# Kernel optimization log

Hardware: AMD Instinct MI355X
Metric: run time of the kernel (lower is better)

## Reference

```python
import jax, jax.numpy as jnp
import numpy as np

N = 50000      # nodes
E_R = 800000   # random edges (plus N self-loops appended)
F = 128        # input feature dim
HD = 256       # base hidden dim
D = 64         # gnn_dim (per-head out channels)
H = 4          # attention heads
A = 32         # n_actions
LEAKY = 0.2    # PyG GATv2 negative_slope default
LN_EPS = 1e-5


def _ln(x, g, b):
    mu = x.mean(-1, keepdims=True)
    v = ((x - mu) ** 2).mean(-1, keepdims=True)
    return (x - mu) / jnp.sqrt(v + LN_EPS) * g + b


def _gatv2(x, src, dst, wl, wr, att, wres, bias):
    # GATv2Conv, concat=False (mean over heads), residual=True, no edge_attr.
    xl = (x @ wl).reshape(-1, H, D)   # [N,H,D] source transform
    xr = (x @ wr).reshape(-1, H, D)   # [N,H,D] target transform
    m = jax.nn.leaky_relu(xl[src] + xr[dst], LEAKY)          # [E,H,D]
    e = jnp.einsum('ehd,hd->eh', m, att)                     # [E,H]
    emax = jax.ops.segment_max(e, dst, num_segments=N)       # [N,H]
    p = jnp.exp(e - emax[dst])
    denom = jax.ops.segment_sum(p, dst, num_segments=N)      # [N,H]
    alpha = p / denom[dst]                                   # segment softmax
    out = jax.ops.segment_sum(alpha[..., None] * xl[src], dst, num_segments=N)
    out = out.mean(axis=1)                                   # concat=False -> head mean
    return out + x @ wres + bias                             # residual + bias


def setup_inputs() -> dict:
    key = jax.random.key(0)
    ks = jax.random.split(key, 16)
    inputs = jax.random.normal(ks[0], (N, F), jnp.float32)
    src_r = jax.random.randint(ks[1], (E_R,), 0, N, jnp.int32)
    dst_r = jax.random.randint(ks[2], (E_R,), 0, N, jnp.int32)
    loops = jnp.arange(N, dtype=jnp.int32)  # add_self_loops=True default in PyG
    src = jnp.concatenate([src_r, loops])
    dst = jnp.concatenate([dst_r, loops])
    w = lambda k, s: jax.random.normal(k, s, jnp.float32) * 0.05
    return {
        'inputs': inputs, 'src': src, 'dst': dst,
        'w0': w(ks[3], (F, HD)), 'b0': jnp.zeros((HD,)), 'g0': jnp.ones((HD,)), 'be0': jnp.zeros((HD,)),
        'w1': w(ks[4], (HD, HD)), 'b1': jnp.zeros((HD,)), 'g1': jnp.ones((HD,)), 'be1': jnp.zeros((HD,)),
        'wl1': w(ks[5], (HD, H * D)), 'wr1': w(ks[6], (HD, H * D)), 'att1': w(ks[7], (H, D)),
        'wres1': w(ks[8], (HD, D)), 'bias1': jnp.zeros((D,)), 'lg1': jnp.ones((D,)), 'lb1': jnp.zeros((D,)),
        'wl2': w(ks[9], (D, H * D)), 'wr2': w(ks[10], (D, H * D)), 'att2': w(ks[11], (H, D)),
        'wres2': w(ks[12], (D, D)), 'bias2': jnp.zeros((D,)), 'lg2': jnp.ones((D,)), 'lb2': jnp.zeros((D,)),
        'wa': w(ks[13], (D, A)), 'ba': jnp.zeros((A,)),
    }


def reference(inputs, src, dst, w0, b0, g0, be0, w1, b1, g1, be1,
              wl1, wr1, att1, wres1, bias1, lg1, lb1,
              wl2, wr2, att2, wres2, bias2, lg2, lb2, wa, ba):
    # base MLP: (Linear + ReLU + LayerNorm) x 2
    x = _ln(jax.nn.relu(inputs @ w0 + b0), g0, be0)
    x = _ln(jax.nn.relu(x @ w1 + b1), g1, be1)
    # GATv2 stack: (GATv2Conv + ReLU + LayerNorm) x 2
    h = _ln(jax.nn.relu(_gatv2(x, src, dst, wl1, wr1, att1, wres1, bias1)), lg1, lb1)
    h = _ln(jax.nn.relu(_gatv2(h, src, dst, wl2, wr2, att2, wres2, bias2)), lg2, lb2)
    q = h @ wa + ba
    return q
```

## Files before the change

### kernel.cpp

```cpp
#include <hip/hip_runtime.h>
#include <stdint.h>

#define LEAKY 0.2f
#define LN_EPS 1e-5f
#define BF16_ONES 0x3F803F80u

extern "C" __global__ void GNNAgentV2_84834194031328_kernel() {}

typedef __attribute__((ext_vector_type(8))) short short8;
typedef __attribute__((ext_vector_type(4))) float f32x4;

__device__ __forceinline__ float bfbits2f(uint32_t bits){
    union { uint32_t u; float f; } c; c.u = bits; return c.f;
}
__device__ __forceinline__ float bf2f(uint16_t u){ return bfbits2f(((uint32_t)u) << 16); }
__device__ __forceinline__ uint16_t f2bf(float f){
    union { float f; uint32_t u; } c; c.f = f;
    uint32_t u = c.u;
    return (uint16_t)((u + 0x7fffu + ((u >> 16) & 1u)) >> 16);
}
__device__ __forceinline__ void ld_bf16x4(const uint16_t* p, float* o){
    uint2 v = *(const uint2*)p;
    o[0] = bfbits2f(v.x << 16);
    o[1] = bfbits2f(v.x & 0xffff0000u);
    o[2] = bfbits2f(v.y << 16);
    o[3] = bfbits2f(v.y & 0xffff0000u);
}
__device__ __forceinline__ void st_bf16x4(uint16_t* p, float a, float b, float c, float d){
    uint2 v;
    v.x = (uint32_t)f2bf(a) | ((uint32_t)f2bf(b) << 16);
    v.y = (uint32_t)f2bf(c) | ((uint32_t)f2bf(d) << 16);
    *(uint2*)p = v;
}

template<int CTRL>
__device__ __forceinline__ float dpp_add(float v){
    int x = __builtin_amdgcn_update_dpp(0, __builtin_bit_cast(int, v), CTRL, 0xF, 0xF, true);
    return v + __builtin_bit_cast(float, x);
}

struct Seg { const void* src; uint16_t* dst; int K; int N; int colOff; };
struct SegTable { Seg s[22]; };

__global__ void k_front(SegTable st, const uint32_t* __restrict__ g0w,
                        const int* __restrict__ dst, int* __restrict__ counts, int E, int nbE,
                        const void* __restrict__ xin, uint16_t* __restrict__ xout, int nin)
{
    int b = blockIdx.x;
    if (b < nbE){
        int e = b * 256 + threadIdx.x;
        if (e < E) atomicAdd(&counts[dst[e]], 1);
        return;
    }
    b -= nbE;
    if (b < 22 * 256){
        int isbf = (*g0w == BF16_ONES) ? 1 : 0;
        Seg sg = st.s[b >> 8];
        int elems = sg.K * sg.N;
        int idx = (b & 255) * 256 + threadIdx.x;
        if (idx >= elems) return;
        float v = isbf ? bf2f(((const uint16_t*)sg.src)[idx]) : ((const float*)sg.src)[idx];
        if (sg.K == 1){
            sg.dst[idx] = f2bf(v);
            return;
        }
        int k = idx / sg.N, c = idx - k * sg.N;
        int cg = sg.colOff + c;
        int ct = cg >> 6, c64 = cg & 63;
        int cf = c64 >> 4, l15 = c64 & 15;
        int kf = k >> 5, r = k & 31;
        int quad = r >> 3, j = r & 7;
        size_t off = (size_t)ct * sg.K * 64 + kf * 2048 + cf * 512 + (quad * 16 + l15) * 8 + j;
        sg.dst[off] = f2bf(v);
        return;
    }
    b -= 22 * 256;
    {
        if (*g0w == BF16_ONES) return;
        int i = b * 256 + threadIdx.x;
        if (i < nin) xout[i] = f2bf(((const float*)xin)[i]);
    }
}

__global__ void k_scan1(const int* __restrict__ counts, int* __restrict__ offs,
                        int* __restrict__ bsums, int n){
    __shared__ int sd[256];
    int t = threadIdx.x;
    int base = blockIdx.x * 1024 + t * 4;
    int v0 = (base + 0 < n) ? counts[base + 0] : 0;
    int v1 = (base + 1 < n) ? counts[base + 1] : 0;
    int v2 = (base + 2 < n) ? counts[base + 2] : 0;
    int v3 = (base + 3 < n) ? counts[base + 3] : 0;
    int tsum = v0 + v1 + v2 + v3;
    sd[t] = tsum;
    __syncthreads();
    for (int off = 1; off < 256; off <<= 1){
        int x = 0;
        if (t >= off) x = sd[t - off];
        __syncthreads();
        sd[t] += x;
        __syncthreads();
    }
    int run = sd[t] - tsum;
    if (base + 0 < n){ offs[base + 0] = run; } run += v0;
    if (base + 1 < n){ offs[base + 1] = run; } run += v1;
    if (base + 2 < n){ offs[base + 2] = run; } run += v2;
    if (base + 3 < n){ offs[base + 3] = run; }
    if (t == 255) bsums[blockIdx.x] = sd[255];
}
__global__ void k_scan23(const int* __restrict__ bsums, int* __restrict__ offs,
                         int* __restrict__ cursor, int n){
    int lane = threadIdx.x & 63;
    int idx = blockIdx.x >> 2;
    int total = 0;
    for (int base = 0; base < idx; base += 64){
        int v = (base + lane < idx) ? bsums[base + lane] : 0;
        v += __shfl_xor(v, 1);  v += __shfl_xor(v, 2);  v += __shfl_xor(v, 4);
        v += __shfl_xor(v, 8);  v += __shfl_xor(v, 16); v += __shfl_xor(v, 32);
        total += v;
    }
    int i = blockIdx.x * 256 + threadIdx.x;
    if (i < n){
        int o = offs[i] + total;
        offs[i] = o;
        cursor[i] = o;
    }
}
__global__ void k_scatter(const int* __restrict__ src, const int* __restrict__ dst,
                          int* __restrict__ cursor, int* __restrict__ csr_src, int E){
    int e = blockIdx.x * 256 + threadIdx.x;
    if (e < E){
        int p = atomicAdd(&cursor[dst[e]], 1);
        csr_src[p] = src[e];
    }
}

template<int K, int CG, bool BIAS_RELU>
__global__ __launch_bounds__(256, 4) void k_gemm(
    const uint16_t* __restrict__ A,
    const uint16_t* __restrict__ Bp,
    const uint16_t* __restrict__ bias,
    uint16_t* __restrict__ o0, int ld0,
    uint16_t* __restrict__ o1, int ld1,
    uint16_t* __restrict__ o2, int ld2,
    int s1, int s2,
    int n,
    const uint32_t* __restrict__ g0w, int want)
{
    if (want >= 0){
        int isbf = (*g0w == BF16_ONES) ? 1 : 0;
        if (isbf != want) return;
    }
    constexpr int PITCH = K + 8;
    __shared__ __align__(16) uint16_t SMEM[64 * PITCH];
    uint16_t* As = SMEM;
    uint16_t* Cs = SMEM;
    int t = threadIdx.x;
    int row0 = blockIdx.x * 64;
    int ctBase = blockIdx.y * CG;

    constexpr int KC = K / 8;
    for (int c = t; c < 64 * KC; c += 256){
        int r = c / KC, kc = c - r * KC;
        uint4 v = make_uint4(0, 0, 0, 0);
        int gr = row0 + r;
        if (gr < n) v = *(const uint4*)(A + (size_t)gr * K + kc * 8);
        *(uint4*)(As + r * PITCH + kc * 8) = v;
    }

    int lane = t & 63, wv = t >> 6;
    int quad = lane >> 4, l15 = lane & 15;
    int wrow = wv * 16;

    __syncthreads();

    constexpr int KF = K / 32;
    short8 areg[KF];
    #pragma unroll
    for (int kf = 0; kf < KF; ++kf)
        areg[kf] = __builtin_bit_cast(short8,
            *(const uint4*)(As + (wrow + l15) * PITCH + kf * 32 + quad * 8));

    __syncthreads();

    for (int g = 0; g < CG; ++g){
        int ct = ctBase + g;
        const uint16_t* Bb = Bp + (size_t)ct * K * 64 + (size_t)lane * 8;

        f32x4 acc[4];
        #pragma unroll
        for (int j = 0; j < 4; ++j) acc[j] = (f32x4){0.f, 0.f, 0.f, 0.f};

        short8 bcur[4], bnxt[4];
        #pragma unroll
        for (int cf = 0; cf < 4; ++cf)
            bcur[cf] = __builtin_bit_cast(short8, *(const uint4*)(Bb + cf * 512));

        #pragma unroll
        for (int kf = 0; kf < KF; ++kf){
            if (kf + 1 < KF){
                #pragma unroll
                for (int cf = 0; cf < 4; ++cf)
                    bnxt[cf] = __builtin_bit_cast(short8,
                        *(const uint4*)(Bb + (kf + 1) * 2048 + cf * 512));
            }
            #pragma unroll
            for (int cf = 0; cf < 4; ++cf)
                acc[cf] = __builtin_amdgcn_mfma_f32_16x16x32_bf16(areg[kf], bcur[cf], acc[cf], 0, 0, 0);
            if (kf + 1 < KF){
                #pragma unroll
                for (int cf = 0; cf < 4; ++cf) bcur[cf] = bnxt[cf];
            }
        }

        #pragma unroll
        for (int r = 0; r < 4; ++r){
            #pragma unroll
            for (int cf = 0; cf < 4; ++cf){
                float v = acc[cf][r];
                if (BIAS_RELU){
                    v += bf2f(bias[ct * 64 + cf * 16 + l15]);
                    v = v > 0.f ? v : 0.f;
                }
                Cs[(wrow + quad * 4 + r) * 72 + cf * 16 + l15] = f2bf(v);
            }
        }
        __syncthreads();

        uint16_t* obase; int ld, colOut;
        if (ct < s1)      { obase = o0; ld = ld0; colOut = ct * 64; }
        else if (ct < s2) { obase = o1; ld = ld1; colOut = (ct - s1) * 64; }
        else              { obase = o2; ld = ld2; colOut = (ct - s2) * 64; }

        for (int i = t; i < 512; i += 256){
            int row = i >> 3, sg = i & 7;
            int grow = row0 + row;
            if (grow < n){
                uint4 v = *(const uint4*)(Cs + row * 72 + sg * 8);
                *(uint4*)(obase + (size_t)grow * ld + colOut + sg * 8) = v;
            }
        }
        __syncthreads();
    }
}

__global__ __launch_bounds__(256) void k_ln256(
    uint16_t* __restrict__ x, const uint16_t* __restrict__ g,
    const uint16_t* __restrict__ be, int n)
{
    int t = threadIdx.x;
    int lane = t & 63, wv = t >> 6;
    int row = blockIdx.x * 8 + wv * 2;
    int c0 = lane * 4;
    float gv[4], bev[4];
    ld_bf16x4(g + c0, gv);
    ld_bf16x4(be + c0, bev);
    #pragma unroll
    for (int rr = 0; rr < 2; ++rr){
        int r = row + rr;
        if (r >= n) continue;
        float v[4];
        ld_bf16x4(x + (size_t)r * 256 + c0, v);
        float s1 = v[0] + v[1] + v[2] + v[3];
        float s2 = v[0]*v[0] + v[1]*v[1] + v[2]*v[2] + v[3]*v[3];
        #pragma unroll
        for (int m = 1; m < 64; m <<= 1){
            s1 += __shfl_xor(s1, m);
            s2 += __shfl_xor(s2, m);
        }
        float mean = s1 * (1.f / 256.f);
        float var  = s2 * (1.f / 256.f) - mean * mean;
        float rstd = rsqrtf(var + LN_EPS);
        st_bf16x4(x + (size_t)r * 256 + c0,
                  (v[0] - mean) * rstd * gv[0] + bev[0],
                  (v[1] - mean) * rstd * gv[1] + bev[1],
                  (v[2] - mean) * rstd * gv[2] + bev[2],
                  (v[3] - mean) * rstd * gv[3] + bev[3]);
    }
}

__global__ __launch_bounds__(128) void k_gat_aggregate(
    const uint16_t* __restrict__ xl, const uint16_t* __restrict__ xr,
    const uint16_t* __restrict__ res,
    const uint16_t* __restrict__ att,
    const uint16_t* __restrict__ bias,
    const uint16_t* __restrict__ lg, const uint16_t* __restrict__ lb,
    const int* __restrict__ offs, const int* __restrict__ counts, const int* __restrict__ csr_src,
    uint16_t* __restrict__ out, int n)
{
    int node = __builtin_amdgcn_readfirstlane((blockIdx.x << 1) + (threadIdx.x >> 6));
    if (node >= n) return;
    int lane = threadIdx.x & 63;
    int c0 = lane * 4;
    float xr4[4], av[4];
    ld_bf16x4(xr + (size_t)node * 256 + c0, xr4);
    ld_bf16x4(att + c0, av);
    int start = offs[node], cnt = counts[node];
    float lsum = 0.f;
    float a0 = 0.f, a1 = 0.f, a2 = 0.f, a3 = 0.f;

    #define EDGE_SCORE(x, e)                                             \
    {                                                                    \
        float u0 = x[0] + xr4[0]; u0 = fmaxf(u0, LEAKY * u0);            \
        float u1 = x[1] + xr4[1]; u1 = fmaxf(u1, LEAKY * u1);            \
        float u2 = x[2] + xr4[2]; u2 = fmaxf(u2, LEAKY * u2);            \
        float u3 = x[3] + xr4[3]; u3 = fmaxf(u3, LEAKY * u3);            \
        e = u0 * av[0] + u1 * av[1] + u2 * av[2] + u3 * av[3];           \
    }
    #define REDUCE16(e)                                                  \
        e = dpp_add<0xB1>(e);                                            \
        e = dpp_add<0x4E>(e);                                            \
        e = dpp_add<0x141>(e);                                           \
        e = dpp_add<0x140>(e);

    int j = 0;
    if (cnt >= 4){
        int i0 = csr_src[start + 0];
        int i1 = csr_src[start + 1];
        int i2 = csr_src[start + 2];
        int i3 = csr_src[start + 3];
        while (true){
            int t0 = __builtin_amdgcn_readfirstlane(i0);
            int t1 = __builtin_amdgcn_readfirstlane(i1);
            int t2 = __builtin_amdgcn_readfirstlane(i2);
            int t3 = __builtin_amdgcn_readfirstlane(i3);
            int jn = j + 4;
            bool more = (jn + 3 < cnt);
            if (more){
                i0 = csr_src[start + jn + 0];
                i1 = csr_src[start + jn + 1];
                i2 = csr_src[start + jn + 2];
                i3 = csr_src[start + jn + 3];
            }
            float x0[4], x1[4], x2[4], x3[4];
            ld_bf16x4(xl + (size_t)(uint32_t)t0 * 256 + c0, x0);
            ld_bf16x4(xl + (size_t)(uint32_t)t1 * 256 + c0, x1);
            ld_bf16x4(xl + (size_t)(uint32_t)t2 * 256 + c0, x2);
            ld_bf16x4(xl + (size_t)(uint32_t)t3 * 256 + c0, x3);
            float e0, e1, e2, e3;
            EDGE_SCORE(x0, e0); EDGE_SCORE(x1, e1); EDGE_SCORE(x2, e2); EDGE_SCORE(x3, e3);
            REDUCE16(e0); REDUCE16(e1); REDUCE16(e2); REDUCE16(e3);
            float p0 = __expf(e0);
            float p1 = __expf(e1);
            float p2 = __expf(e2);
            float p3 = __expf(e3);
            a0 += p0*x0[0] + p1*x1[0] + p2*x2[0] + p3*x3[0];
            a1 += p0*x0[1] + p1*x1[1] + p2*x2[1] + p3*x3[1];
            a2 += p0*x0[2] + p1*x1[2] + p2*x2[2] + p3*x3[2];
            a3 += p0*x0[3] + p1*x1[3] + p2*x2[3] + p3*x3[3];
            lsum += p0 + p1 + p2 + p3;
            j = jn;
            if (!more) break;
        }
    }
    for (; j < cnt; ++j){
        int t0 = __builtin_amdgcn_readfirstlane(csr_src[start + j]);
        float x0[4];
        ld_bf16x4(xl + (size_t)(uint32_t)t0 * 256 + c0, x0);
        float e0;
        EDGE_SCORE(x0, e0);
        REDUCE16(e0);
        float p0 = __expf(e0);
        a0 += p0 * x0[0];
        a1 += p0 * x0[1];
        a2 += p0 * x0[2];
        a3 += p0 * x0[3];
        lsum += p0;
    }
    #undef EDGE_SCORE
    #undef REDUCE16

    float inv = 1.f / lsum;
    a0 *= inv; a1 *= inv; a2 *= inv; a3 *= inv;
    a0 += __shfl_xor(a0, 16); a0 += __shfl_xor(a0, 32);
    a1 += __shfl_xor(a1, 16); a1 += __shfl_xor(a1, 32);
    a2 += __shfl_xor(a2, 16); a2 += __shfl_xor(a2, 32);
    a3 += __shfl_xor(a3, 16); a3 += __shfl_xor(a3, 32);
    a0 *= 0.25f; a1 *= 0.25f; a2 *= 0.25f; a3 *= 0.25f;
    int d0 = (lane & 15) * 4;
    float r4[4], bvv[4];
    ld_bf16x4(res + (size_t)node * 64 + d0, r4);
    ld_bf16x4(bias + d0, bvv);
    float v0 = a0 + r4[0] + bvv[0]; v0 = v0 > 0.f ? v0 : 0.f;
    float v1 = a1 + r4[1] + bvv[1]; v1 = v1 > 0.f ? v1 : 0.f;
    float v2 = a2 + r4[2] + bvv[2]; v2 = v2 > 0.f ? v2 : 0.f;
    float v3 = a3 + r4[3] + bvv[3]; v3 = v3 > 0.f ? v3 : 0.f;
    float s1 = v0 + v1 + v2 + v3;
    float s2 = v0*v0 + v1*v1 + v2*v2 + v3*v3;
    s1 += __shfl_xor(s1, 1); s2 += __shfl_xor(s2, 1);
    s1 += __shfl_xor(s1, 2); s2 += __shfl_xor(s2, 2);
    s1 += __shfl_xor(s1, 4); s2 += __shfl_xor(s2, 4);
    s1 += __shfl_xor(s1, 8); s2 += __shfl_xor(s2, 8);
    float mean = s1 * (1.f / 64.f);
    float var  = s2 * (1.f / 64.f) - mean * mean;
    float rstd = rsqrtf(var + LN_EPS);
    if (lane < 16){
        float gvv[4], bev[4];
        ld_bf16x4(lg + d0, gvv);
        ld_bf16x4(lb + d0, bev);
        st_bf16x4(out + (size_t)node * 64 + d0,
                  (v0 - mean) * rstd * gvv[0] + bev[0],
                  (v1 - mean) * rstd * gvv[1] + bev[1],
                  (v2 - mean) * rstd * gvv[2] + bev[2],
                  (v3 - mean) * rstd * gvv[3] + bev[3]);
    }
}

__global__ __launch_bounds__(256) void k_final(
    const uint16_t* __restrict__ h, const void* __restrict__ wa,
    const void* __restrict__ ba, void* __restrict__ out, int n,
    const uint32_t* __restrict__ g0w)
{
    __shared__ float was[64][32];
    __shared__ float bas[32];
    __shared__ float hs[8][64];
    int t = threadIdx.x;
    int isbf = (*g0w == BF16_ONES) ? 1 : 0;
    for (int i = t; i < 64 * 32; i += 256)
        was[i >> 5][i & 31] = isbf ? bf2f(((const uint16_t*)wa)[i]) : ((const float*)wa)[i];
    if (t < 32) bas[t] = isbf ? bf2f(((const uint16_t*)ba)[t]) : ((const float*)ba)[t];
    int row0 = blockIdx.x * 8;
    for (int i = t; i < 8 * 64; i += 256){
        int r = i >> 6, k = i & 63;
        int rr = row0 + r;
        hs[r][k] = (rr < n) ? bf2f(h[(size_t)rr * 64 + k]) : 0.f;
    }
    __syncthreads();
    int r = t >> 5, c = t & 31;
    float acc = bas[c];
    #pragma unroll
    for (int k = 0; k < 64; ++k) acc += hs[r][k] * was[k][c];
    int node = row0 + r;
    if (node < n){
        if (isbf) ((uint16_t*)out)[(size_t)node * 32 + c] = f2bf(acc);
        else      ((float*)out)[(size_t)node * 32 + c] = acc;
    }
}

extern "C" void kernel_launch(void* const* d_in, const int* in_sizes, int n_in,
                              void* d_out, int out_size, void* d_ws, size_t ws_size,
                              hipStream_t stream)
{
    const int* src = (const int*)d_in[1];
    const int* dst = (const int*)d_in[2];
    const uint32_t* g0w = (const uint32_t*)d_in[5];
    const int N = in_sizes[0] / 128;
    const int E = in_sizes[1];

    char* base = (char*)d_ws;
    size_t off = 0;
    auto alloc = [&](size_t bytes) -> void* {
        void* p = base + off;
        off += (bytes + 255) & ~(size_t)255;
        return p;
    };
    uint16_t* XIN  = (uint16_t*)alloc((size_t)N * 128 * 2);
    uint16_t* X0   = (uint16_t*)alloc((size_t)N * 256 * 2);
    uint16_t* X1   = (uint16_t*)alloc((size_t)N * 256 * 2);
    uint16_t* XL   = (uint16_t*)alloc((size_t)N * 256 * 2);
    uint16_t* XR   = (uint16_t*)alloc((size_t)N * 256 * 2);
    uint16_t* RES  = (uint16_t*)alloc((size_t)N * 64 * 2);
    uint16_t* w0P  = (uint16_t*)alloc(256 * 128 * 2);
    uint16_t* w1P  = (uint16_t*)alloc(256 * 256 * 2);
    uint16_t* wt1P = (uint16_t*)alloc(576 * 256 * 2);
    uint16_t* wt2P = (uint16_t*)alloc(576 * 64 * 2);
    uint16_t* VEC  = (uint16_t*)alloc(4096 * 2);
    int* counts    = (int*)alloc((size_t)N * 4);
    int* offs      = (int*)alloc((size_t)N * 4);
    int* cursor    = (int*)alloc((size_t)N * 4);
    int* bsums     = (int*)alloc(4096);
    int* csr_src   = (int*)alloc((size_t)E * 4);

    uint16_t* H1 = X0;
    uint16_t* H2 = X0 + (size_t)N * 64;

    const int vB0=0, vG0=256, vBE0=512, vB1=768, vG1=1024, vBE1=1280;
    const int vATT1=1536, vBIAS1=1792, vLG1=1856, vLB1=1920;
    const int vATT2=1984, vBIAS2=2240, vLG2=2304, vLB2=2368;

    SegTable st;
    int si = 0;
    auto seg = [&](int i, uint16_t* d, int K, int Nn, int colOff){
        st.s[si++] = { d_in[i], d, K, Nn, colOff };
    };
    seg(3,  w0P, 128, 256, 0);
    seg(7,  w1P, 256, 256, 0);
    seg(11, wt1P, 256, 256, 0);
    seg(12, wt1P, 256, 256, 256);
    seg(14, wt1P, 256, 64, 512);
    seg(18, wt2P, 64, 256, 0);
    seg(19, wt2P, 64, 256, 256);
    seg(21, wt2P, 64, 64, 512);
    seg(4,  VEC+vB0, 1, 256, 0);  seg(5,  VEC+vG0, 1, 256, 0);  seg(6,  VEC+vBE0, 1, 256, 0);
    seg(8,  VEC+vB1, 1, 256, 0);  seg(9,  VEC+vG1, 1, 256, 0);  seg(10, VEC+vBE1, 1, 256, 0);
    seg(13, VEC+vATT1, 1, 256, 0); seg(15, VEC+vBIAS1, 1, 64, 0);
    seg(16, VEC+vLG1, 1, 64, 0);   seg(17, VEC+vLB1, 1, 64, 0);
    seg(20, VEC+vATT2, 1, 256, 0); seg(22, VEC+vBIAS2, 1, 64, 0);
    seg(23, VEC+vLG2, 1, 64, 0);   seg(24, VEC+vLB2, 1, 64, 0);

    const int nin = N * 128;
    const int nbE = (E + 255) / 256;
    const int nbI = (nin + 255) / 256;
    const int nb_scan  = (N + 1023) / 1024;
    const int nb_nodes = (N + 255) / 256;

    hipMemsetAsync(counts, 0, (size_t)N * 4, stream);
    k_front<<<nbE + 22 * 256 + nbI, 256, 0, stream>>>(
        st, g0w, dst, counts, E, nbE, d_in[0], XIN, nin);

    k_scan1<<<nb_scan, 256, 0, stream>>>(counts, offs, bsums, N);
    k_scan23<<<nb_nodes, 256, 0, stream>>>(bsums, offs, cursor, N);
    k_scatter<<<nbE, 256, 0, stream>>>(src, dst, cursor, csr_src, E);

    const int rt = (N + 63) / 64;
    const int nb_ln  = (N + 7) / 8;
    const int nb_agg = (N + 1) / 2;

    k_gemm<128, 4, true><<<rt, 256, 0, stream>>>(
        (const uint16_t*)d_in[0], w0P, VEC+vB0, X0,256, X0,256, X0,256, 99, 99, N, g0w, 1);
    k_gemm<128, 4, true><<<rt, 256, 0, stream>>>(
        XIN, w0P, VEC+vB0, X0,256, X0,256, X0,256, 99, 99, N, g0w, 0);
    k_ln256<<<nb_ln, 256, 0, stream>>>(X0, VEC+vG0, VEC+vBE0, N);
    k_gemm<256, 4, true><<<rt, 256, 0, stream>>>(
        X0, w1P, VEC+vB1, X1,256, X1,256, X1,256, 99, 99, N, nullptr, -1);
    k_ln256<<<nb_ln, 256, 0, stream>>>(X1, VEC+vG1, VEC+vBE1, N);

    k_gemm<256, 9, false><<<rt, 256, 0, stream>>>(
        X1, wt1P, nullptr, XL,256, XR,256, RES,64, 4, 8, N, nullptr, -1);
    k_gat_aggregate<<<nb_agg, 128, 0, stream>>>(XL, XR, RES,
        VEC+vATT1, VEC+vBIAS1, VEC+vLG1, VEC+vLB1, offs, counts, csr_src, H1, N);

    k_gemm<64, 9, false><<<rt, 256, 0, stream>>>(
        H1, wt2P, nullptr, XL,256, XR,256, RES,64, 4, 8, N, nullptr, -1);
    k_gat_aggregate<<<nb_agg, 128, 0, stream>>>(XL, XR, RES,
        VEC+vATT2, VEC+vBIAS2, VEC+vLG2, VEC+vLB2, offs, counts, csr_src, H2, N);

    k_final<<<nb_ln, 256, 0, stream>>>(H2, d_in[25], d_in[26], d_out, N, g0w);
}
```

Measured before the change: 497.0 us.

## Store GAT projections as fp16 and compute edge scores with packed fp16 dot2

The projection GEMMs now write XL/XR/RES in fp16 instead of bf16. The aggregation kernel computes leaky-relu and the attention dot product with packed half2 math and fdot2. In the 4-edge loop, the four per-edge 16-lane reductions are merged into one DPP transpose-and-reduce, so a single exp serves all four edges, and the results are broadcast back with DPP quad permutes. This is meant to cut VALU work and DPP and exp instruction count in the latency-bound gather loop. In exchange it loses range relative to bf16, which risks overflow if projected values get large.

Result: faster. 485.0 us (-2.4%).

```diff
diff --git a/kernel.cpp b/kernel.cpp
--- a/kernel.cpp
+++ b/kernel.cpp
@@ -9,6 +9,7 @@
 
 typedef __attribute__((ext_vector_type(8))) short short8;
 typedef __attribute__((ext_vector_type(4))) float f32x4;
+typedef _Float16 f16x2 __attribute__((ext_vector_type(2)));
 
 __device__ __forceinline__ float bfbits2f(uint32_t bits){
     union { uint32_t u; float f; } c; c.u = bits; return c.f;
@@ -19,6 +20,11 @@
     uint32_t u = c.u;
     return (uint16_t)((u + 0x7fffu + ((u >> 16) & 1u)) >> 16);
 }
+__device__ __forceinline__ uint16_t f2h(float f){
+    _Float16 h = (_Float16)f;
+    return __builtin_bit_cast(uint16_t, h);
+}
+__device__ __forceinline__ f16x2 u2h2(uint32_t u){ return __builtin_bit_cast(f16x2, u); }
 __device__ __forceinline__ void ld_bf16x4(const uint16_t* p, float* o){
     uint2 v = *(const uint2*)p;
     o[0] = bfbits2f(v.x << 16);
@@ -33,10 +39,24 @@
     *(uint2*)p = v;
 }
 
+__device__ __forceinline__ float dot2acc(f16x2 a, f16x2 b, float c){
+#if __has_builtin(__builtin_amdgcn_fdot2)
+    return __builtin_amdgcn_fdot2(a, b, c, false);
+#else
+    c = fmaf((float)a.x, (float)b.x, c);
+    return fmaf((float)a.y, (float)b.y, c);
+#endif
+}
+
 template<int CTRL>
 __device__ __forceinline__ float dpp_add(float v){
     int x = __builtin_amdgcn_update_dpp(0, __builtin_bit_cast(int, v), CTRL, 0xF, 0xF, true);
     return v + __builtin_bit_cast(float, x);
+}
+template<int CTRL>
+__device__ __forceinline__ float dpp_mov(float v){
+    int x = __builtin_amdgcn_update_dpp(0, __builtin_bit_cast(int, v), CTRL, 0xF, 0xF, true);
+    return __builtin_bit_cast(float, x);
 }
 
 struct Seg { const void* src; uint16_t* dst; int K; int N; int colOff; };
@@ -135,7 +155,7 @@
     }
 }
 
-template<int K, int CG, bool BIAS_RELU>
+template<int K, int CG, bool BIAS_RELU, bool OUT_F16>
 __global__ __launch_bounds__(256, 4) void k_gemm(
     const uint16_t* __restrict__ A,
     const uint16_t* __restrict__ Bp,
@@ -222,7 +242,7 @@
                     v += bf2f(bias[ct * 64 + cf * 16 + l15]);
                     v = v > 0.f ? v : 0.f;
                 }
-                Cs[(wrow + quad * 4 + r) * 72 + cf * 16 + l15] = f2bf(v);
+                Cs[(wrow + quad * 4 + r) * 72 + cf * 16 + l15] = OUT_F16 ? f2h(v) : f2bf(v);
             }
         }
         __syncthreads();
@@ -292,26 +312,25 @@
     if (node >= n) return;
     int lane = threadIdx.x & 63;
     int c0 = lane * 4;
-    float xr4[4], av[4];
-    ld_bf16x4(xr + (size_t)node * 256 + c0, xr4);
+    uint2 xrv = *(const uint2*)(xr + (size_t)node * 256 + c0);
+    f16x2 xr0 = u2h2(xrv.x), xr1 = u2h2(xrv.y);
+    float av[4];
     ld_bf16x4(att + c0, av);
+    f16x2 av0 = { (_Float16)av[0], (_Float16)av[1] };
+    f16x2 av1 = { (_Float16)av[2], (_Float16)av[3] };
+    const f16x2 lk2 = { (_Float16)LEAKY, (_Float16)LEAKY };
+    bool par1 = (lane & 1) != 0, par2 = (lane & 2) != 0;
     int start = offs[node], cnt = counts[node];
     float lsum = 0.f;
     float a0 = 0.f, a1 = 0.f, a2 = 0.f, a3 = 0.f;
 
-    #define EDGE_SCORE(x, e)                                             \
+    #define EDGE_SCORE_H(xa, xb, e)                                      \
     {                                                                    \
-        float u0 = x[0] + xr4[0]; u0 = fmaxf(u0, LEAKY * u0);            \
-        float u1 = x[1] + xr4[1]; u1 = fmaxf(u1, LEAKY * u1);            \
-        float u2 = x[2] + xr4[2]; u2 = fmaxf(u2, LEAKY * u2);            \
-        float u3 = x[3] + xr4[3]; u3 = fmaxf(u3, LEAKY * u3);            \
-        e = u0 * av[0] + u1 * av[1] + u2 * av[2] + u3 * av[3];           \
-    }
-    #define REDUCE16(e)                                                  \
-        e = dpp_add<0xB1>(e);                                            \
-        e = dpp_add<0x4E>(e);                                            \
-        e = dpp_add<0x141>(e);                                           \
-        e = dpp_add<0x140>(e);
+        f16x2 u0 = xa + xr0, u1 = xb + xr1;                              \
+        f16x2 m0 = __builtin_elementwise_max(u0, u0 * lk2);              \
+        f16x2 m1 = __builtin_elementwise_max(u1, u1 * lk2);              \
+        e = dot2acc(m0, av0, dot2acc(m1, av1, 0.f));                     \
+    }
 
     int j = 0;
     if (cnt >= 4){
@@ -332,43 +351,58 @@
                 i2 = csr_src[start + jn + 2];
                 i3 = csr_src[start + jn + 3];
             }
-            float x0[4], x1[4], x2[4], x3[4];
-            ld_bf16x4(xl + (size_t)(uint32_t)t0 * 256 + c0, x0);
-            ld_bf16x4(xl + (size_t)(uint32_t)t1 * 256 + c0, x1);
-            ld_bf16x4(xl + (size_t)(uint32_t)t2 * 256 + c0, x2);
-            ld_bf16x4(xl + (size_t)(uint32_t)t3 * 256 + c0, x3);
+            f16x2 x0a, x0b, x1a, x1b, x2a, x2b, x3a, x3b;
+            { uint2 v = *(const uint2*)(xl + (size_t)(uint32_t)t0 * 256 + c0); x0a = u2h2(v.x); x0b = u2h2(v.y); }
+            { uint2 v = *(const uint2*)(xl + (size_t)(uint32_t)t1 * 256 + c0); x1a = u2h2(v.x); x1b = u2h2(v.y); }
+            { uint2 v = *(const uint2*)(xl + (size_t)(uint32_t)t2 * 256 + c0); x2a = u2h2(v.x); x2b = u2h2(v.y); }
+            { uint2 v = *(const uint2*)(xl + (size_t)(uint32_t)t3 * 256 + c0); x3a = u2h2(v.x); x3b = u2h2(v.y); }
             float e0, e1, e2, e3;
-            EDGE_SCORE(x0, e0); EDGE_SCORE(x1, e1); EDGE_SCORE(x2, e2); EDGE_SCORE(x3, e3);
-            REDUCE16(e0); REDUCE16(e1); REDUCE16(e2); REDUCE16(e3);
-            float p0 = __expf(e0);
-            float p1 = __expf(e1);
-            float p2 = __expf(e2);
-            float p3 = __expf(e3);
-            a0 += p0*x0[0] + p1*x1[0] + p2*x2[0] + p3*x3[0];
-            a1 += p0*x0[1] + p1*x1[1] + p2*x2[1] + p3*x3[1];
-            a2 += p0*x0[2] + p1*x1[2] + p2*x2[2] + p3*x3[2];
-            a3 += p0*x0[3] + p1*x1[3] + p2*x2[3] + p3*x3[3];
-            lsum += p0 + p1 + p2 + p3;
+            EDGE_SCORE_H(x0a, x0b, e0); EDGE_SCORE_H(x1a, x1b, e1);
+            EDGE_SCORE_H(x2a, x2b, e2); EDGE_SCORE_H(x3a, x3b, e3);
+            float b01 = par1 ? e0 : e1;
+            float z01 = (par1 ? e1 : e0) + dpp_mov<0xB1>(b01);
+            float b23 = par1 ? e2 : e3;
+            float z23 = (par1 ? e3 : e2) + dpp_mov<0xB1>(b23);
+            float bz = par2 ? z01 : z23;
+            float z  = (par2 ? z23 : z01) + dpp_mov<0x4E>(bz);
+            z += dpp_mov<0x124>(z);
+            z += dpp_mov<0x128>(z);
+            float pz = __expf(z);
+            float p0 = dpp_mov<0x00>(pz);
+            float p1 = dpp_mov<0x55>(pz);
+            float p2 = dpp_mov<0xAA>(pz);
+            float p3 = dpp_mov<0xFF>(pz);
+            a0 = fmaf((float)x0a.x, p0, a0); a0 = fmaf((float)x1a.x, p1, a0);
+            a0 = fmaf((float)x2a.x, p2, a0); a0 = fmaf((float)x3a.x, p3, a0);
+            a1 = fmaf((float)x0a.y, p0, a1); a1 = fmaf((float)x1a.y, p1, a1);
+            a1 = fmaf((float)x2a.y, p2, a1); a1 = fmaf((float)x3a.y, p3, a1);
+            a2 = fmaf((float)x0b.x, p0, a2); a2 = fmaf((float)x1b.x, p1, a2);
+            a2 = fmaf((float)x2b.x, p2, a2); a2 = fmaf((float)x3b.x, p3, a2);
+            a3 = fmaf((float)x0b.y, p0, a3); a3 = fmaf((float)x1b.y, p1, a3);
+            a3 = fmaf((float)x2b.y, p2, a3); a3 = fmaf((float)x3b.y, p3, a3);
+            lsum += (p0 + p1) + (p2 + p3);
             j = jn;
             if (!more) break;
         }
     }
     for (; j < cnt; ++j){
         int t0 = __builtin_amdgcn_readfirstlane(csr_src[start + j]);
-        float x0[4];
-        ld_bf16x4(xl + (size_t)(uint32_t)t0 * 256 + c0, x0);
+        uint2 v = *(const uint2*)(xl + (size_t)(uint32_t)t0 * 256 + c0);
+        f16x2 xa = u2h2(v.x), xb = u2h2(v.y);
         float e0;
-        EDGE_SCORE(x0, e0);
-        REDUCE16(e0);
+        EDGE_SCORE_H(xa, xb, e0);
+        e0 = dpp_add<0xB1>(e0);
+        e0 = dpp_add<0x4E>(e0);
+        e0 = dpp_add<0x141>(e0);
+        e0 = dpp_add<0x140>(e0);
         float p0 = __expf(e0);
-        a0 += p0 * x0[0];
-        a1 += p0 * x0[1];
-        a2 += p0 * x0[2];
-        a3 += p0 * x0[3];
+        a0 = fmaf((float)xa.x, p0, a0);
+        a1 = fmaf((float)xa.y, p0, a1);
+        a2 = fmaf((float)xb.x, p0, a2);
+        a3 = fmaf((float)xb.y, p0, a3);
         lsum += p0;
     }
-    #undef EDGE_SCORE
-    #undef REDUCE16
+    #undef EDGE_SCORE_H
 
     float inv = 1.f / lsum;
     a0 *= inv; a1 *= inv; a2 *= inv; a3 *= inv;
@@ -378,13 +412,14 @@
     a3 += __shfl_xor(a3, 16); a3 += __shfl_xor(a3, 32);
     a0 *= 0.25f; a1 *= 0.25f; a2 *= 0.25f; a3 *= 0.25f;
     int d0 = (lane & 15) * 4;
-    float r4[4], bvv[4];
-    ld_bf16x4(res + (size_t)node * 64 + d0, r4);
+    uint2 rv = *(const uint2*)(res + (size_t)node * 64 + d0);
+    f16x2 r01 = u2h2(rv.x), r23 = u2h2(rv.y);
+    float bvv[4];
     ld_bf16x4(bias + d0, bvv);
-    float v0 = a0 + r4[0] + bvv[0]; v0 = v0 > 0.f ? v0 : 0.f;
-    float v1 = a1 + r4[1] + bvv[1]; v1 = v1 > 0.f ? v1 : 0.f;
-    float v2 = a2 + r4[2] + bvv[2]; v2 = v2 > 0.f ? v2 : 0.f;
-    float v3 = a3 + r4[3] + bvv[3]; v3 = v3 > 0.f ? v3 : 0.f;
+    float v0 = a0 + (float)r01.x + bvv[0]; v0 = v0 > 0.f ? v0 : 0.f;
+    float v1 = a1 + (float)r01.y + bvv[1]; v1 = v1 > 0.f ? v1 : 0.f;
+    float v2 = a2 + (float)r23.x + bvv[2]; v2 = v2 > 0.f ? v2 : 0.f;
+    float v3 = a3 + (float)r23.y + bvv[3]; v3 = v3 > 0.f ? v3 : 0.f;
     float s1 = v0 + v1 + v2 + v3;
     float s2 = v0*v0 + v1*v1 + v2*v2 + v3*v3;
     s1 += __shfl_xor(s1, 1); s2 += __shfl_xor(s2, 1);
@@ -516,21 +551,21 @@
     const int nb_ln  = (N + 7) / 8;
     const int nb_agg = (N + 1) / 2;
 
-    k_gemm<128, 4, true><<<rt, 256, 0, stream>>>(
+    k_gemm<128, 4, true, false><<<rt, 256, 0, stream>>>(
         (const uint16_t*)d_in[0], w0P, VEC+vB0, X0,256, X0,256, X0,256, 99, 99, N, g0w, 1);
-    k_gemm<128, 4, true><<<rt, 256, 0, stream>>>(
+    k_gemm<128, 4, true, false><<<rt, 256, 0, stream>>>(
         XIN, w0P, VEC+vB0, X0,256, X0,256, X0,256, 99, 99, N, g0w, 0);
     k_ln256<<<nb_ln, 256, 0, stream>>>(X0, VEC+vG0, VEC+vBE0, N);
-    k_gemm<256, 4, true><<<rt, 256, 0, stream>>>(
+    k_gemm<256, 4, true, false><<<rt, 256, 0, stream>>>(
         X0, w1P, VEC+vB1, X1,256, X1,256, X1,256, 99, 99, N, nullptr, -1);
     k_ln256<<<nb_ln, 256, 0, stream>>>(X1, VEC+vG1, VEC+vBE1, N);
 
-    k_gemm<256, 9, false><<<rt, 256, 0, stream>>>(
+    k_gemm<256, 9, false, true><<<rt, 256, 0, stream>>>(
         X1, wt1P, nullptr, XL,256, XR,256, RES,64, 4, 8, N, nullptr, -1);
     k_gat_aggregate<<<nb_agg, 128, 0, stream>>>(XL, XR, RES,
         VEC+vATT1, VEC+vBIAS1, VEC+vLG1, VEC+vLB1, offs, counts, csr_src, H1, N);
 
-    k_gemm<64, 9, false><<<rt, 256, 0, stream>>>(
+    k_gemm<64, 9, false, true><<<rt, 256, 0, stream>>>(
         H1, wt2P, nullptr, XL,256, XR,256, RES,64, 4, 8, N, nullptr, -1);
     k_gat_aggregate<<<nb_agg, 128, 0, stream>>>(XL, XR, RES,
         VEC+vATT2, VEC+vBIAS2, VEC+vLG2, VEC+vLB2, offs, counts, csr_src, H2, N);
```
